# Kernel tuning notes

Measured on AMD Instinct MI355X. Metric: run time of the kernel, lower is better.

## Reference

```python
import jax, jax.numpy as jnp
import numpy as np

N_HOPS = 2
LEAKY_SLOPE = 0.2
EPS = 1e-12


def setup_inputs() -> dict:
    key = jax.random.key(0)
    k1, k2, k3, k4, k5, k6 = jax.random.split(key, 6)
    N, R, C, E = 100000, 50, 64, 1000000
    return {
        "entity_emb": jax.random.normal(k1, (N, C), dtype=jnp.float32) * 0.1,
        "relation_emb": jax.random.normal(k2, (R, C), dtype=jnp.float32) * 0.1,
        "fc_w": jax.random.normal(k3, (C, 2 * C), dtype=jnp.float32) * 0.1,  # torch Linear weight [out, in]
        "fc_b": jax.random.normal(k4, (C,), dtype=jnp.float32) * 0.1,
        "edge_index": jax.random.randint(k5, (2, E), 0, N, dtype=jnp.int64),
        "edge_type": jax.random.randint(k6, (E,), 0, R, dtype=jnp.int64),
    }


def reference(entity_emb, relation_emb, fc_w, fc_b, edge_index, edge_type):
    """RGAT.forward with mess_dropout=False: n_hops of relational-attention
    gather -> leakyrelu -> scatter_softmax(head) -> scatter_sum -> residual -> L2 normalize."""
    N = entity_emb.shape[0]
    head, tail = edge_index[0], edge_index[1]
    rel_e = relation_emb[edge_type]  # [E, C]

    def agg(emb):
        a_input = jnp.concatenate([emb[head], emb[tail]], axis=-1)  # [E, 2C]
        h = a_input @ fc_w.T + fc_b                                  # fc(a_input): [E, C]
        e = jnp.sum(h * rel_e, axis=-1)                              # [E]
        e = jnp.where(e > 0, e, LEAKY_SLOPE * e)                     # leakyrelu(0.2)
        # scatter_softmax over head segments (numerically stable)
        m = jax.ops.segment_max(e, head, num_segments=N)             # [N]
        ex = jnp.exp(e - m[head])
        denom = jax.ops.segment_sum(ex, head, num_segments=N)        # [N]
        w = ex / denom[head]                                         # [E]
        agg_emb = jax.ops.segment_sum(emb[tail] * w[:, None], head, num_segments=N)
        agg_emb = agg_emb + emb                                      # residual
        return agg_emb

    emb = entity_emb
    for _ in range(N_HOPS):
        emb = agg(emb)
        # F.normalize(emb): L2 along dim=1 with eps clamp
        nrm = jnp.sqrt(jnp.sum(emb * emb, axis=-1, keepdims=True))
        emb = emb / jnp.maximum(nrm, EPS)
    return emb
```

## Files before the change

### kernel.cpp

```cpp
#include <hip/hip_runtime.h>

#define C 64
#define RMAX 50
#define LEAKY 0.2f
#define CAP 48

__device__ __forceinline__ float bf2f(unsigned short u) {
  return __uint_as_float(((unsigned)u) << 16);
}
__device__ __forceinline__ unsigned short f2bf(float x) {
  unsigned u = __float_as_uint(x);
  return (unsigned short)((u + 0x7FFFu + ((u >> 16) & 1u)) >> 16);
}

__device__ __forceinline__ int wave_isbf(const void* ent) {
  const unsigned* w = (const unsigned*)ent;
  const int lane = threadIdx.x & 63;
  int ok = 0;
#pragma unroll
  for (int i = 0; i < 4; ++i) {
    unsigned lo = w[lane + 64 * i] & 0xFFFFu;
    float a = fabsf(__uint_as_float(lo << 16));
    ok += (lo == 0u || (a >= 1e-9f && a <= 1e9f)) ? 1 : 0;
  }
#pragma unroll
  for (int d = 1; d < 64; d <<= 1) ok += __shfl_xor(ok, d, 64);
  return ok >= 224;
}
__device__ __forceinline__ int wave_is64(const int* p) {
  const int lane = threadIdx.x & 63;
  int z = (p[2 * lane + 1] == 0) ? 1 : 0;
#pragma unroll
  for (int d = 1; d < 64; d <<= 1) z += __shfl_xor(z, d, 64);
  return z >= 62;
}
__device__ __forceinline__ float loadF(const void* p, int i, int isbf) {
  return isbf ? bf2f(((const unsigned short*)p)[i]) : ((const float*)p)[i];
}

__global__ void uvc_kernel(const void* __restrict__ rel,
                           const void* __restrict__ fcw,
                           const void* __restrict__ fcb,
                           float* __restrict__ U, float* __restrict__ V,
                           float* __restrict__ cvec) {
  const int isbf = wave_isbf(rel);
  const int r = blockIdx.x;
  const int i = threadIdx.x;
  float acc = 0.f;
  for (int o = 0; o < C; ++o)
    acc += loadF(rel, r * C + o, isbf) * loadF(fcw, o * (2 * C) + i, isbf);
  if (i < C) U[r * C + i] = acc;
  else       V[r * C + (i - C)] = acc;
  if (i < C) {
    float p = loadF(rel, r * C + i, isbf) * loadF(fcb, i, isbf);
#pragma unroll
    for (int d = 1; d < 64; d <<= 1) p += __shfl_xor(p, d, 64);
    if (i == 0) cvec[r] = p;
  }
}

__global__ void conv_kernel(const void* __restrict__ ent, unsigned* __restrict__ dst,
                            int n8) {
  const int isbf = wave_isbf(ent);
  int i = blockIdx.x * blockDim.x + threadIdx.x;
  if (i >= n8) return;
  uint4 o;
  if (isbf) {
    o = ((const uint4*)ent)[i];
  } else {
    const float4* q = (const float4*)ent;
    float4 a = q[2 * i], b = q[2 * i + 1];
    o.x = (unsigned)f2bf(a.x) | ((unsigned)f2bf(a.y) << 16);
    o.y = (unsigned)f2bf(a.z) | ((unsigned)f2bf(a.w) << 16);
    o.z = (unsigned)f2bf(b.x) | ((unsigned)f2bf(b.y) << 16);
    o.w = (unsigned)f2bf(b.z) | ((unsigned)f2bf(b.w) << 16);
  }
  ((uint4*)dst)[i] = o;
}

__global__ void fillb_kernel(const int* __restrict__ eidx, const int* __restrict__ etype,
                             int* __restrict__ cnt, int* __restrict__ packed,
                             int E, int N, int Rc) {
  const int is64 = wave_is64(eidx);
  const int et64 = wave_is64(etype);
  const int base = (blockIdx.x * blockDim.x + threadIdx.x) * 4;
  int h[4], t[4], r[4];
#pragma unroll
  for (int k = 0; k < 4; ++k) {
    const int e = base + k;
    if (e < E) {
      h[k] = is64 ? eidx[2 * e] : eidx[e];
      t[k] = is64 ? eidx[2 * E + 2 * e] : eidx[E + e];
      r[k] = et64 ? etype[2 * e] : etype[e];
    }
  }
  int pos[4];
#pragma unroll
  for (int k = 0; k < 4; ++k) {
    const int e = base + k;
    if (e < E) {
      if ((unsigned)h[k] >= (unsigned)N) h[k] = 0;
      pos[k] = atomicAdd(&cnt[h[k]], 1);
    }
  }
#pragma unroll
  for (int k = 0; k < 4; ++k) {
    const int e = base + k;
    if (e < E && pos[k] < CAP) {
      int tt = t[k]; if ((unsigned)tt >= (unsigned)N) tt = 0;
      int rr = r[k]; if ((unsigned)rr >= (unsigned)Rc) rr = 0;
      packed[h[k] * CAP + pos[k]] = tt | (rr << 20);
    }
  }
}

template <bool PACK4>
__global__ void fillA_kernel(const int* __restrict__ eidx, const int* __restrict__ etype,
                             int* __restrict__ bcnt, int* __restrict__ bbuf,
                             int E, int N, int Rc, int shift, int nbuck, int bcap) {
  __shared__ int lh[256];
  __shared__ int gbase[256];
  const int is64 = wave_is64(eidx);
  const int et64 = wave_is64(etype);
  const int tid = threadIdx.x;
  if (tid < 256) lh[tid] = 0;
  const int eBase = blockIdx.x * 1024;
  int h[4], tr[4], bk[4], lp[4], ok[4];
  __syncthreads();
#pragma unroll
  for (int k = 0; k < 4; ++k) {
    const int e = eBase + k * 256 + tid;
    ok[k] = (e < E);
    if (ok[k]) {
      int hh = is64 ? eidx[2 * e] : eidx[e];
      int tt = is64 ? eidx[2 * E + 2 * e] : eidx[E + e];
      int rr = et64 ? etype[2 * e] : etype[e];
      if ((unsigned)hh >= (unsigned)N) hh = 0;
      if ((unsigned)tt >= (unsigned)N) tt = 0;
      if ((unsigned)rr >= (unsigned)Rc) rr = 0;
      h[k] = hh;
      if (PACK4) tr[k] = ((hh & 511) << 23) | (rr << 17) | tt;
      else       tr[k] = tt | (rr << 20);
      bk[k] = hh >> shift;
      lp[k] = atomicAdd(&lh[bk[k]], 1);
    }
  }
  __syncthreads();
  if (tid < nbuck) gbase[tid] = lh[tid] ? atomicAdd(&bcnt[tid * 16], lh[tid]) : 0;
  __syncthreads();
#pragma unroll
  for (int k = 0; k < 4; ++k) {
    if (ok[k]) {
      int posb = gbase[bk[k]] + lp[k];
      if (posb < bcap) {
        if (PACK4) bbuf[(size_t)bk[k] * bcap + posb] = tr[k];
        else ((int2*)bbuf)[(size_t)bk[k] * bcap + posb] = make_int2(h[k], tr[k]);
      }
    }
  }
}

template <bool PACK4>
__global__ void fillB_kernel(const int* __restrict__ bcnt, const int* __restrict__ bbuf,
                             int* __restrict__ cnt, int* __restrict__ packed,
                             int N, int bcap, int shift) {
  const int b = blockIdx.x;
  int bc = bcnt[b * 16]; if (bc > bcap) bc = bcap;
  for (int k = threadIdx.x; k < bc; k += blockDim.x) {
    int h, pk;
    if (PACK4) {
      unsigned w = (unsigned)bbuf[(size_t)b * bcap + k];
      h = (b << shift) | (int)(w >> 23);
      int t = (int)(w & 0x1FFFFu);
      int r = (int)((w >> 17) & 63u);
      pk = t | (r << 20);
    } else {
      int2 e = ((const int2*)bbuf)[(size_t)b * bcap + k];
      h = e.x; pk = e.y;
    }
    if ((unsigned)h >= (unsigned)N) h = 0;
    int pos = atomicAdd(&cnt[h], 1);
    if (pos < CAP) packed[h * CAP + pos] = pk;
  }
}

__global__ void histo_kernel(const int* __restrict__ cnt, int* __restrict__ hist, int N) {
  __shared__ int histS[65];
  const int tid = threadIdx.x;
  for (int k = tid; k < 65; k += 1024) histS[k] = 0;
  __syncthreads();
  const int i = blockIdx.x * 1024 + tid;
  if (i < N) {
    int b = cnt[i]; if (b > 64) b = 64;
    atomicAdd(&histS[b], 1);
  }
  __syncthreads();
  for (int k = tid; k < 65; k += 1024)
    if (histS[k]) atomicAdd(&hist[k * 16], histS[k]);
}

__global__ void order_kernel(const int* __restrict__ cnt, const int* __restrict__ hist,
                             int* __restrict__ bincur, int* __restrict__ order, int N) {
  __shared__ int binstart[66];
  __shared__ int lh[65];
  __shared__ int lbase[65];
  const int tid = threadIdx.x;
  for (int k = tid; k < 65; k += 1024) { binstart[k] = hist[k * 16]; lh[k] = 0; }
  __syncthreads();
  if (tid == 0) {
    int run = 0;
    for (int k = 64; k >= 0; --k) { int t = binstart[k]; binstart[k] = run; run += t; }
    binstart[65] = run;
  }
  __syncthreads();
  const int i = blockIdx.x * 1024 + tid;
  int b = 0, lpos = 0;
  if (i < N) {
    b = cnt[i]; if (b > 64) b = 64;
    lpos = atomicAdd(&lh[b], 1);
  }
  __syncthreads();
  if (tid < 65) lbase[tid] = lh[tid] ? atomicAdd(&bincur[tid * 16], lh[tid]) : 0;
  __syncthreads();
  if (i < N) {
    int dst = binstart[b] + lbase[b] + lpos;
    if ((unsigned)dst < (unsigned)N) order[dst] = i;
  }
}

__device__ __forceinline__ void unpack8(uint4 u, float4& a, float4& b) {
  a.x = __uint_as_float(u.x << 16); a.y = __uint_as_float(u.x & 0xFFFF0000u);
  a.z = __uint_as_float(u.y << 16); a.w = __uint_as_float(u.y & 0xFFFF0000u);
  b.x = __uint_as_float(u.z << 16); b.y = __uint_as_float(u.z & 0xFFFF0000u);
  b.z = __uint_as_float(u.w << 16); b.w = __uint_as_float(u.w & 0xFFFF0000u);
}

template <bool IN_EXT, bool OUT_EXT>
__global__ __launch_bounds__(256) void hop_kernel(
    const void* __restrict__ emb_in_v, void* __restrict__ emb_out_v,
    const int* __restrict__ cnt, const int* __restrict__ packed,
    const float* __restrict__ Ug, const float* __restrict__ Vg,
    const float* __restrict__ cg, const int* __restrict__ order,
    const void* __restrict__ ent_det, int N, int Rc) {
  int isbf = 1;
  if (IN_EXT || OUT_EXT) isbf = wave_isbf(ent_det);
  const int l = threadIdx.x & 7;
  const int slot = blockIdx.x * 32 + (threadIdx.x >> 3);
  if (slot >= N) return;
  const int n = order[slot];

  auto loadRow = [&](int row, float4& a, float4& b) {
    if (IN_EXT && !isbf) {
      const float4* q = (const float4*)((const float*)emb_in_v + (size_t)row * C);
      a = q[2 * l]; b = q[2 * l + 1];
    } else {
      uint4 u = ((const uint4*)emb_in_v)[(size_t)row * 8 + l];
      unpack8(u, a, b);
    }
  };

  const int start = n * CAP;
  int deg = cnt[n];
  if (deg > CAP) deg = CAP;
  if (deg < 0) deg = 0;

  float4 enA, enB;
  loadRow(n, enA, enB);

  float sum = 0.f;
  float4 accA = {0.f, 0.f, 0.f, 0.f}, accB = {0.f, 0.f, 0.f, 0.f};

  int4 pk = (deg > 0) ? *(const int4*)&packed[start] : make_int4(0, 0, 0, 0);
  for (int j0 = 0; j0 < deg; j0 += 4) {
    const int4 cur = pk;
    if (j0 + 4 < deg) pk = *(const int4*)&packed[start + j0 + 4];

    int tt[4], rr[4];
    tt[0] = cur.x & 0xFFFFF; rr[0] = (int)((unsigned)cur.x >> 20);
    tt[1] = cur.y & 0xFFFFF; rr[1] = (int)((unsigned)cur.y >> 20);
    tt[2] = cur.z & 0xFFFFF; rr[2] = (int)((unsigned)cur.z >> 20);
    tt[3] = cur.w & 0xFFFFF; rr[3] = (int)((unsigned)cur.w >> 20);
#pragma unroll
    for (int k = 0; k < 4; ++k) {
      if (tt[k] >= N) tt[k] = 0;
      if (rr[k] >= Rc) rr[k] = 0;
    }
    float4 eA[4], eB[4];
#pragma unroll
    for (int k = 0; k < 4; ++k) loadRow(tt[k], eA[k], eB[k]);
    float4 uA[4], uB[4], vA[4], vB[4];
    float cbv[4];
#pragma unroll
    for (int k = 0; k < 4; ++k) {
      const float4* uq = (const float4*)&Ug[rr[k] * C + l * 8];
      const float4* vq = (const float4*)&Vg[rr[k] * C + l * 8];
      uA[k] = uq[0]; uB[k] = uq[1];
      vA[k] = vq[0]; vB[k] = vq[1];
      cbv[k] = cg[rr[k]];
    }
#pragma unroll
    for (int k = 0; k < 4; ++k) {
      float p = uA[k].x * enA.x + uA[k].y * enA.y + uA[k].z * enA.z + uA[k].w * enA.w
              + uB[k].x * enB.x + uB[k].y * enB.y + uB[k].z * enB.z + uB[k].w * enB.w
              + vA[k].x * eA[k].x + vA[k].y * eA[k].y + vA[k].z * eA[k].z + vA[k].w * eA[k].w
              + vB[k].x * eB[k].x + vB[k].y * eB[k].y + vB[k].z * eB[k].z + vB[k].w * eB[k].w;
      p += __shfl_xor(p, 1); p += __shfl_xor(p, 2); p += __shfl_xor(p, 4);
      float s = p + cbv[k];
      s = s > 0.f ? s : LEAKY * s;
      const float wgt = (j0 + k < deg) ? __expf(fminf(s, 50.f)) : 0.f;
      sum += wgt;
      accA.x += wgt * eA[k].x; accA.y += wgt * eA[k].y;
      accA.z += wgt * eA[k].z; accA.w += wgt * eA[k].w;
      accB.x += wgt * eB[k].x; accB.y += wgt * eB[k].y;
      accB.z += wgt * eB[k].z; accB.w += wgt * eB[k].w;
    }
  }

  const float inv = (deg > 0) ? 1.0f / sum : 0.f;
  float4 oA, oB;
  oA.x = accA.x * inv + enA.x; oA.y = accA.y * inv + enA.y;
  oA.z = accA.z * inv + enA.z; oA.w = accA.w * inv + enA.w;
  oB.x = accB.x * inv + enB.x; oB.y = accB.y * inv + enB.y;
  oB.z = accB.z * inv + enB.z; oB.w = accB.w * inv + enB.w;

  float ss = oA.x * oA.x + oA.y * oA.y + oA.z * oA.z + oA.w * oA.w
           + oB.x * oB.x + oB.y * oB.y + oB.z * oB.z + oB.w * oB.w;
  ss += __shfl_xor(ss, 1); ss += __shfl_xor(ss, 2); ss += __shfl_xor(ss, 4);
  const float sc = 1.0f / fmaxf(sqrtf(ss), 1e-12f);
  oA.x *= sc; oA.y *= sc; oA.z *= sc; oA.w *= sc;
  oB.x *= sc; oB.y *= sc; oB.z *= sc; oB.w *= sc;

  if (OUT_EXT && !isbf) {
    float4* q = (float4*)((float*)emb_out_v + (size_t)n * C);
    q[2 * l] = oA; q[2 * l + 1] = oB;
  } else {
    uint4 u;
    u.x = (unsigned)f2bf(oA.x) | ((unsigned)f2bf(oA.y) << 16);
    u.y = (unsigned)f2bf(oA.z) | ((unsigned)f2bf(oA.w) << 16);
    u.z = (unsigned)f2bf(oB.x) | ((unsigned)f2bf(oB.y) << 16);
    u.w = (unsigned)f2bf(oB.z) | ((unsigned)f2bf(oB.w) << 16);
    ((uint4*)emb_out_v)[(size_t)n * 8 + l] = u;
  }
}

extern "C" void kernel_launch(void* const* d_in, const int* in_sizes, int n_in,
                              void* d_out, int out_size, void* d_ws, size_t ws_size,
                              hipStream_t stream) {
  const void* ent  = d_in[0];
  const void* rel  = d_in[1];
  const void* fcw  = d_in[2];
  const void* fcb  = d_in[3];
  const int* eidx  = (const int*)d_in[4];
  const int* etype = (const int*)d_in[5];

  const int N  = in_sizes[0] / C;
  const int R0 = in_sizes[1] / C;
  const int Rc = R0 < RMAX ? R0 : RMAX;
  const int E  = in_sizes[5];
  const int nbN = (N + 1023) / 1024;
  (void)n_in; (void)out_size;

  int shift = 9;
  while ((((N - 1) >> shift) + 1) > 256) shift++;
  const int nbuck = ((N - 1) >> shift) + 1;
  int bcap = (E + nbuck - 1) / nbuck;
  bcap += bcap / 4 + 256;
  const bool pack4 = (N <= 131072) && (Rc <= 64) && (shift == 9);

  char* ws = (char*)d_ws;
  size_t off = 0;
  auto alloc = [&](size_t bytes) -> void* {
    void* p = ws + off;
    off = (off + bytes + 255) & ~(size_t)255;
    return p;
  };
  const int zwords = N + 1040 + 1040 + 4096 + 64;
  int*   cnt    = (int*)alloc((size_t)zwords * 4);
  int*   hist   = cnt + N;
  int*   bincur = hist + 1040;
  int*   bcnt   = bincur + 1040;
  float* U      = (float*)alloc((size_t)Rc * C * 4);
  float* V      = (float*)alloc((size_t)Rc * C * 4);
  float* cv     = (float*)alloc((size_t)Rc * 4);
  int*   order  = (int*)alloc((size_t)N * 4);
  int*   packed = (int*)alloc((size_t)N * CAP * 4);
  const size_t emb0B   = (size_t)N * C * 2;
  const size_t bucketB = (size_t)nbuck * bcap * (pack4 ? 4 : 8);
  const size_t midB    = (size_t)N * C * 2;
  const size_t base    = off;
  const size_t align = 256;
  const bool tier2 = base + ((emb0B > bucketB ? emb0B : bucketB) + align) + (midB + align) <= ws_size;

  void* unionbuf = alloc(tier2 ? (emb0B > bucketB ? emb0B : bucketB) : 0);
  unsigned short* mid = (unsigned short*)alloc(midB);
  unsigned short* emb0 = (unsigned short*)unionbuf;
  int* bbuf = (int*)unionbuf;

  hipMemsetAsync(cnt, 0, (size_t)zwords * 4, stream);
  uvc_kernel<<<Rc, 128, 0, stream>>>(rel, fcw, fcb, U, V, cv);

  const int hb = (N + 31) / 32;
  if (tier2) {
    if (pack4) {
      fillA_kernel<true ><<<(E + 1023) / 1024, 256, 0, stream>>>(eidx, etype, bcnt, bbuf,
                                                                 E, N, Rc, shift, nbuck, bcap);
      fillB_kernel<true ><<<nbuck, 512, 0, stream>>>(bcnt, bbuf, cnt, packed, N, bcap, shift);
    } else {
      fillA_kernel<false><<<(E + 1023) / 1024, 256, 0, stream>>>(eidx, etype, bcnt, bbuf,
                                                                 E, N, Rc, shift, nbuck, bcap);
      fillB_kernel<false><<<nbuck, 512, 0, stream>>>(bcnt, bbuf, cnt, packed, N, bcap, shift);
    }
    histo_kernel<<<nbN, 1024, 0, stream>>>(cnt, hist, N);
    order_kernel<<<nbN, 1024, 0, stream>>>(cnt, hist, bincur, order, N);
    const int n8 = N * C / 8;
    conv_kernel<<<(n8 + 255) / 256, 256, 0, stream>>>(ent, (unsigned*)emb0, n8);
    hop_kernel<false, false><<<hb, 256, 0, stream>>>(emb0, mid, cnt, packed, U, V, cv, order, ent, N, Rc);
  } else {
    fillb_kernel<<<(E + 1023) / 1024, 256, 0, stream>>>(eidx, etype, cnt, packed, E, N, Rc);
    histo_kernel<<<nbN, 1024, 0, stream>>>(cnt, hist, N);
    order_kernel<<<nbN, 1024, 0, stream>>>(cnt, hist, bincur, order, N);
    hop_kernel<true,  false><<<hb, 256, 0, stream>>>(ent, mid, cnt, packed, U, V, cv, order, ent, N, Rc);
  }
  hop_kernel<false, true ><<<hb, 256, 0, stream>>>(mid, d_out, cnt, packed, U, V, cv, order, ent, N, Rc);
}
```

Baseline: 238.1 us.

## Fuse preprocessing kernels to cut launch count and add nontemporal output stores

Folds the relation U/V/c precompute and the zeroing of the count arrays into extra blocks of the edge-bucketing kernel. Merges the degree histogram into the bucket scatter kernel and the ordering pass into the bf16 conversion kernel. This cuts the number of launches and small serial kernels in the setup chain. The final-hop output now uses nontemporal stores. One risk: zeroing cnt inside fillA relies on fillB's atomics running only after fillA completes, which stream ordering provides.

```diff
diff --git a/kernel.cpp b/kernel.cpp
--- a/kernel.cpp
+++ b/kernel.cpp
@@ -5,6 +5,8 @@
 #define LEAKY 0.2f
 #define CAP 48
 
+typedef unsigned uvec4 __attribute__((ext_vector_type(4)));
+
 __device__ __forceinline__ float bf2f(unsigned short u) {
   return __uint_as_float(((unsigned)u) << 16);
 }
@@ -38,91 +40,40 @@
   return isbf ? bf2f(((const unsigned short*)p)[i]) : ((const float*)p)[i];
 }
 
-__global__ void uvc_kernel(const void* __restrict__ rel,
-                           const void* __restrict__ fcw,
-                           const void* __restrict__ fcb,
-                           float* __restrict__ U, float* __restrict__ V,
-                           float* __restrict__ cvec) {
-  const int isbf = wave_isbf(rel);
-  const int r = blockIdx.x;
-  const int i = threadIdx.x;
-  float acc = 0.f;
-  for (int o = 0; o < C; ++o)
-    acc += loadF(rel, r * C + o, isbf) * loadF(fcw, o * (2 * C) + i, isbf);
-  if (i < C) U[r * C + i] = acc;
-  else       V[r * C + (i - C)] = acc;
-  if (i < C) {
-    float p = loadF(rel, r * C + i, isbf) * loadF(fcb, i, isbf);
-#pragma unroll
-    for (int d = 1; d < 64; d <<= 1) p += __shfl_xor(p, d, 64);
-    if (i == 0) cvec[r] = p;
-  }
-}
-
-__global__ void conv_kernel(const void* __restrict__ ent, unsigned* __restrict__ dst,
-                            int n8) {
-  const int isbf = wave_isbf(ent);
-  int i = blockIdx.x * blockDim.x + threadIdx.x;
-  if (i >= n8) return;
-  uint4 o;
-  if (isbf) {
-    o = ((const uint4*)ent)[i];
-  } else {
-    const float4* q = (const float4*)ent;
-    float4 a = q[2 * i], b = q[2 * i + 1];
-    o.x = (unsigned)f2bf(a.x) | ((unsigned)f2bf(a.y) << 16);
-    o.y = (unsigned)f2bf(a.z) | ((unsigned)f2bf(a.w) << 16);
-    o.z = (unsigned)f2bf(b.x) | ((unsigned)f2bf(b.y) << 16);
-    o.w = (unsigned)f2bf(b.z) | ((unsigned)f2bf(b.w) << 16);
-  }
-  ((uint4*)dst)[i] = o;
-}
-
-__global__ void fillb_kernel(const int* __restrict__ eidx, const int* __restrict__ etype,
-                             int* __restrict__ cnt, int* __restrict__ packed,
-                             int E, int N, int Rc) {
-  const int is64 = wave_is64(eidx);
-  const int et64 = wave_is64(etype);
-  const int base = (blockIdx.x * blockDim.x + threadIdx.x) * 4;
-  int h[4], t[4], r[4];
-#pragma unroll
-  for (int k = 0; k < 4; ++k) {
-    const int e = base + k;
-    if (e < E) {
-      h[k] = is64 ? eidx[2 * e] : eidx[e];
-      t[k] = is64 ? eidx[2 * E + 2 * e] : eidx[E + e];
-      r[k] = et64 ? etype[2 * e] : etype[e];
-    }
-  }
-  int pos[4];
-#pragma unroll
-  for (int k = 0; k < 4; ++k) {
-    const int e = base + k;
-    if (e < E) {
-      if ((unsigned)h[k] >= (unsigned)N) h[k] = 0;
-      pos[k] = atomicAdd(&cnt[h[k]], 1);
-    }
-  }
-#pragma unroll
-  for (int k = 0; k < 4; ++k) {
-    const int e = base + k;
-    if (e < E && pos[k] < CAP) {
-      int tt = t[k]; if ((unsigned)tt >= (unsigned)N) tt = 0;
-      int rr = r[k]; if ((unsigned)rr >= (unsigned)Rc) rr = 0;
-      packed[h[k] * CAP + pos[k]] = tt | (rr << 20);
-    }
-  }
-}
-
 template <bool PACK4>
 __global__ void fillA_kernel(const int* __restrict__ eidx, const int* __restrict__ etype,
                              int* __restrict__ bcnt, int* __restrict__ bbuf,
-                             int E, int N, int Rc, int shift, int nbuck, int bcap) {
+                             int E, int N, int Rc, int shift, int nbuck, int bcap,
+                             int faBlocks, int* __restrict__ zbase, int zwords,
+                             const void* __restrict__ rel, const void* __restrict__ fcw,
+                             const void* __restrict__ fcb,
+                             float* __restrict__ U, float* __restrict__ V,
+                             float* __restrict__ cvec) {
+  const int tid = threadIdx.x;
+  if (blockIdx.x >= faBlocks) {
+    const int r = blockIdx.x - faBlocks;
+    const int isbf = wave_isbf(rel);
+    if (tid < 128) {
+      float acc = 0.f;
+      for (int o = 0; o < C; ++o)
+        acc += loadF(rel, r * C + o, isbf) * loadF(fcw, o * (2 * C) + tid, isbf);
+      if (tid < C) U[r * C + tid] = acc;
+      else         V[r * C + (tid - C)] = acc;
+      if (tid < C) {
+        float p = loadF(rel, r * C + tid, isbf) * loadF(fcb, tid, isbf);
+#pragma unroll
+        for (int d = 1; d < 64; d <<= 1) p += __shfl_xor(p, d, 64);
+        if (tid == 0) cvec[r] = p;
+      }
+    }
+    return;
+  }
+  for (int i = blockIdx.x * 256 + tid; i < zwords; i += faBlocks * 256) zbase[i] = 0;
+
   __shared__ int lh[256];
   __shared__ int gbase[256];
   const int is64 = wave_is64(eidx);
   const int et64 = wave_is64(etype);
-  const int tid = threadIdx.x;
   if (tid < 256) lh[tid] = 0;
   const int eBase = blockIdx.x * 1024;
   int h[4], tr[4], bk[4], lp[4], ok[4];
@@ -163,10 +114,13 @@
 template <bool PACK4>
 __global__ void fillB_kernel(const int* __restrict__ bcnt, const int* __restrict__ bbuf,
                              int* __restrict__ cnt, int* __restrict__ packed,
-                             int N, int bcap, int shift) {
+                             int N, int bcap, int shift, int* __restrict__ hist) {
+  __shared__ int histS[65];
   const int b = blockIdx.x;
+  const int tid = threadIdx.x;
+  for (int k = tid; k < 65; k += blockDim.x) histS[k] = 0;
   int bc = bcnt[b * 16]; if (bc > bcap) bc = bcap;
-  for (int k = threadIdx.x; k < bc; k += blockDim.x) {
+  for (int k = tid; k < bc; k += blockDim.x) {
     int h, pk;
     if (PACK4) {
       unsigned w = (unsigned)bbuf[(size_t)b * bcap + k];
@@ -182,8 +136,119 @@
     int pos = atomicAdd(&cnt[h], 1);
     if (pos < CAP) packed[h * CAP + pos] = pk;
   }
-}
-
+  __syncthreads();
+  const int h0 = b << shift;
+  const int h1 = min(N, (b + 1) << shift);
+  for (int h = h0 + tid; h < h1; h += blockDim.x) {
+    int d = cnt[h]; if (d > 64) d = 64;
+    atomicAdd(&histS[d], 1);
+  }
+  __syncthreads();
+  for (int k = tid; k < 65; k += blockDim.x)
+    if (histS[k]) atomicAdd(&hist[k * 16], histS[k]);
+}
+
+__global__ void conv_order_kernel(const void* __restrict__ ent, unsigned* __restrict__ dst,
+                                  int n8, const int* __restrict__ cnt,
+                                  const int* __restrict__ hist, int* __restrict__ bincur,
+                                  int* __restrict__ order, int N, int nbOrd) {
+  __shared__ int binstart[66];
+  __shared__ int lh[65];
+  __shared__ int lbase[65];
+  const int tid = threadIdx.x;
+  if (blockIdx.x < nbOrd) {
+    for (int k = tid; k < 65; k += 256) { binstart[k] = hist[k * 16]; lh[k] = 0; }
+    __syncthreads();
+    if (tid == 0) {
+      int run = 0;
+      for (int k = 64; k >= 0; --k) { int t = binstart[k]; binstart[k] = run; run += t; }
+      binstart[65] = run;
+    }
+    __syncthreads();
+    const int i = blockIdx.x * 256 + tid;
+    int b = 0, lpos = 0;
+    if (i < N) {
+      b = cnt[i]; if (b > 64) b = 64;
+      lpos = atomicAdd(&lh[b], 1);
+    }
+    __syncthreads();
+    if (tid < 65) lbase[tid] = lh[tid] ? atomicAdd(&bincur[tid * 16], lh[tid]) : 0;
+    __syncthreads();
+    if (i < N) {
+      int dst2 = binstart[b] + lbase[b] + lpos;
+      if ((unsigned)dst2 < (unsigned)N) order[dst2] = i;
+    }
+  }
+  const int isbf = wave_isbf(ent);
+  const int gid = blockIdx.x * 256 + tid;
+  if (gid >= n8) return;
+  uint4 o;
+  if (isbf) {
+    o = ((const uint4*)ent)[gid];
+  } else {
+    const float4* q = (const float4*)ent;
+    float4 a = q[2 * gid], b2 = q[2 * gid + 1];
+    o.x = (unsigned)f2bf(a.x) | ((unsigned)f2bf(a.y) << 16);
+    o.y = (unsigned)f2bf(a.z) | ((unsigned)f2bf(a.w) << 16);
+    o.z = (unsigned)f2bf(b2.x) | ((unsigned)f2bf(b2.y) << 16);
+    o.w = (unsigned)f2bf(b2.z) | ((unsigned)f2bf(b2.w) << 16);
+  }
+  ((uint4*)dst)[gid] = o;
+}
+
+__global__ void fillb_kernel(const int* __restrict__ eidx, const int* __restrict__ etype,
+                             int* __restrict__ cnt, int* __restrict__ packed,
+                             int E, int N, int Rc) {
+  const int is64 = wave_is64(eidx);
+  const int et64 = wave_is64(etype);
+  const int base = (blockIdx.x * blockDim.x + threadIdx.x) * 4;
+  int h[4], t[4], r[4];
+#pragma unroll
+  for (int k = 0; k < 4; ++k) {
+    const int e = base + k;
+    if (e < E) {
+      h[k] = is64 ? eidx[2 * e] : eidx[e];
+      t[k] = is64 ? eidx[2 * E + 2 * e] : eidx[E + e];
+      r[k] = et64 ? etype[2 * e] : etype[e];
+    }
+  }
+  int pos[4];
+#pragma unroll
+  for (int k = 0; k < 4; ++k) {
+    const int e = base + k;
+    if (e < E) {
+      if ((unsigned)h[k] >= (unsigned)N) h[k] = 0;
+      pos[k] = atomicAdd(&cnt[h[k]], 1);
+    }
+  }
+#pragma unroll
+  for (int k = 0; k < 4; ++k) {
+    const int e = base + k;
+    if (e < E && pos[k] < CAP) {
+      int tt = t[k]; if ((unsigned)tt >= (unsigned)N) tt = 0;
+      int rr = r[k]; if ((unsigned)rr >= (unsigned)Rc) rr = 0;
+      packed[h[k] * CAP + pos[k]] = tt | (rr << 20);
+    }
+  }
+}
+__global__ void uvc_kernel(const void* __restrict__ rel, const void* __restrict__ fcw,
+                           const void* __restrict__ fcb, float* __restrict__ U,
+                           float* __restrict__ V, float* __restrict__ cvec) {
+  const int isbf = wave_isbf(rel);
+  const int r = blockIdx.x;
+  const int i = threadIdx.x;
+  float acc = 0.f;
+  for (int o = 0; o < C; ++o)
+    acc += loadF(rel, r * C + o, isbf) * loadF(fcw, o * (2 * C) + i, isbf);
+  if (i < C) U[r * C + i] = acc;
+  else       V[r * C + (i - C)] = acc;
+  if (i < C) {
+    float p = loadF(rel, r * C + i, isbf) * loadF(fcb, i, isbf);
+#pragma unroll
+    for (int d = 1; d < 64; d <<= 1) p += __shfl_xor(p, d, 64);
+    if (i == 0) cvec[r] = p;
+  }
+}
 __global__ void histo_kernel(const int* __restrict__ cnt, int* __restrict__ hist, int N) {
   __shared__ int histS[65];
   const int tid = threadIdx.x;
@@ -198,7 +263,6 @@
   for (int k = tid; k < 65; k += 1024)
     if (histS[k]) atomicAdd(&hist[k * 16], histS[k]);
 }
-
 __global__ void order_kernel(const int* __restrict__ cnt, const int* __restrict__ hist,
                              int* __restrict__ bincur, int* __restrict__ order, int N) {
   __shared__ int binstart[66];
@@ -331,15 +395,21 @@
   oB.x *= sc; oB.y *= sc; oB.z *= sc; oB.w *= sc;
 
   if (OUT_EXT && !isbf) {
-    float4* q = (float4*)((float*)emb_out_v + (size_t)n * C);
-    q[2 * l] = oA; q[2 * l + 1] = oB;
+    float* q = (float*)emb_out_v + (size_t)n * C + l * 8;
+    uvec4 w0 = { __float_as_uint(oA.x), __float_as_uint(oA.y),
+                 __float_as_uint(oA.z), __float_as_uint(oA.w) };
+    uvec4 w1 = { __float_as_uint(oB.x), __float_as_uint(oB.y),
+                 __float_as_uint(oB.z), __float_as_uint(oB.w) };
+    __builtin_nontemporal_store(w0, (uvec4*)q);
+    __builtin_nontemporal_store(w1, (uvec4*)(q + 4));
   } else {
-    uint4 u;
-    u.x = (unsigned)f2bf(oA.x) | ((unsigned)f2bf(oA.y) << 16);
-    u.y = (unsigned)f2bf(oA.z) | ((unsigned)f2bf(oA.w) << 16);
-    u.z = (unsigned)f2bf(oB.x) | ((unsigned)f2bf(oB.y) << 16);
-    u.w = (unsigned)f2bf(oB.z) | ((unsigned)f2bf(oB.w) << 16);
-    ((uint4*)emb_out_v)[(size_t)n * 8 + l] = u;
+    uvec4 u = { (unsigned)f2bf(oA.x) | ((unsigned)f2bf(oA.y) << 16),
+                (unsigned)f2bf(oA.z) | ((unsigned)f2bf(oA.w) << 16),
+                (unsigned)f2bf(oB.x) | ((unsigned)f2bf(oB.y) << 16),
+                (unsigned)f2bf(oB.z) | ((unsigned)f2bf(oB.w) << 16) };
+    uvec4* dst = (uvec4*)((unsigned short*)emb_out_v + (size_t)n * C) + l;
+    if (OUT_EXT) __builtin_nontemporal_store(u, dst);
+    else *dst = u;
   }
 }
 
@@ -374,8 +444,8 @@
     off = (off + bytes + 255) & ~(size_t)255;
     return p;
   };
-  const int zwords = N + 1040 + 1040 + 4096 + 64;
-  int*   cnt    = (int*)alloc((size_t)zwords * 4);
+  const int zwords = N + 1040 + 1040;
+  int*   cnt    = (int*)alloc((size_t)(zwords + 4096 + 64) * 4);
   int*   hist   = cnt + N;
   int*   bincur = hist + 1040;
   int*   bcnt   = bincur + 1040;
@@ -396,26 +466,31 @@
   unsigned short* emb0 = (unsigned short*)unionbuf;
   int* bbuf = (int*)unionbuf;
 
-  hipMemsetAsync(cnt, 0, (size_t)zwords * 4, stream);
-  uvc_kernel<<<Rc, 128, 0, stream>>>(rel, fcw, fcb, U, V, cv);
-
   const int hb = (N + 31) / 32;
   if (tier2) {
-    if (pack4) {
-      fillA_kernel<true ><<<(E + 1023) / 1024, 256, 0, stream>>>(eidx, etype, bcnt, bbuf,
-                                                                 E, N, Rc, shift, nbuck, bcap);
-      fillB_kernel<true ><<<nbuck, 512, 0, stream>>>(bcnt, bbuf, cnt, packed, N, bcap, shift);
-    } else {
-      fillA_kernel<false><<<(E + 1023) / 1024, 256, 0, stream>>>(eidx, etype, bcnt, bbuf,
-                                                                 E, N, Rc, shift, nbuck, bcap);
-      fillB_kernel<false><<<nbuck, 512, 0, stream>>>(bcnt, bbuf, cnt, packed, N, bcap, shift);
-    }
-    histo_kernel<<<nbN, 1024, 0, stream>>>(cnt, hist, N);
-    order_kernel<<<nbN, 1024, 0, stream>>>(cnt, hist, bincur, order, N);
+    hipMemsetAsync(bcnt, 0, (size_t)(4096 + 64) * 4, stream);
+    const int fa = (E + 1023) / 1024;
+    if (pack4)
+      fillA_kernel<true ><<<fa + Rc, 256, 0, stream>>>(eidx, etype, bcnt, bbuf, E, N, Rc,
+                                                       shift, nbuck, bcap, fa, cnt, zwords,
+                                                       rel, fcw, fcb, U, V, cv);
+    else
+      fillA_kernel<false><<<fa + Rc, 256, 0, stream>>>(eidx, etype, bcnt, bbuf, E, N, Rc,
+                                                       shift, nbuck, bcap, fa, cnt, zwords,
+                                                       rel, fcw, fcb, U, V, cv);
+    if (pack4)
+      fillB_kernel<true ><<<nbuck, 512, 0, stream>>>(bcnt, bbuf, cnt, packed, N, bcap, shift, hist);
+    else
+      fillB_kernel<false><<<nbuck, 512, 0, stream>>>(bcnt, bbuf, cnt, packed, N, bcap, shift, hist);
     const int n8 = N * C / 8;
-    conv_kernel<<<(n8 + 255) / 256, 256, 0, stream>>>(ent, (unsigned*)emb0, n8);
+    const int cb = (n8 + 255) / 256;
+    const int nbOrd = (N + 255) / 256;
+    conv_order_kernel<<<cb, 256, 0, stream>>>(ent, (unsigned*)emb0, n8, cnt, hist,
+                                              bincur, order, N, nbOrd);
     hop_kernel<false, false><<<hb, 256, 0, stream>>>(emb0, mid, cnt, packed, U, V, cv, order, ent, N, Rc);
   } else {
+    hipMemsetAsync(cnt, 0, (size_t)(zwords + 4096 + 64) * 4, stream);
+    uvc_kernel<<<Rc, 128, 0, stream>>>(rel, fcw, fcb, U, V, cv);
     fillb_kernel<<<(E + 1023) / 1024, 256, 0, stream>>>(eidx, etype, cnt, packed, E, N, Rc);
     histo_kernel<<<nbN, 1024, 0, stream>>>(cnt, hist, N);
     order_kernel<<<nbN, 1024, 0, stream>>>(cnt, hist, bincur, order, N);
```

New measurement: 230.7 us. -3.1%, faster.
